# Kernel optimization log

Hardware: AMD Instinct MI355X
Metric: run time of the kernel (lower is better)

Reference implementation:

```python
import jax, jax.numpy as jnp
import numpy as np

B, QLEN, MLEN, E, H, DH = 2, 1024, 1024, 1024, 16, 64
KLEN = QLEN + MLEN
LN_EPS = 1e-3  # keras LayerNormalization default epsilon


def layer_norm(x, gamma, beta):
    mu = jnp.mean(x, axis=-1, keepdims=True)
    var = jnp.mean(jnp.square(x - mu), axis=-1, keepdims=True)
    return (x - mu) * jax.lax.rsqrt(var + LN_EPS) * gamma + beta


def rel_shift(x):
    # x: [B, H, q, k] -> standard Transformer-XL relative shift
    b, h, q, k = x.shape
    x = jnp.pad(x, ((0, 0), (0, 0), (0, 0), (1, 0)))
    x = x.reshape(b, h, k + 1, q)[:, :, 1:, :]
    return x.reshape(b, h, q, k)


def setup_inputs() -> dict:
    key = jax.random.key(0)
    ks = jax.random.split(key, 12)
    s = 0.02
    inp = {
        "w": jax.random.normal(ks[0], (B, QLEN, E), jnp.float32),
        "r": jax.random.normal(ks[1], (1, KLEN, E), jnp.float32),
        "member": jax.random.normal(ks[2], (B, MLEN, E), jnp.float32),
        # causal mask over concatenated keys: 1 = masked
        "attn_mask": (jnp.arange(KLEN)[None, :] > (jnp.arange(QLEN)[:, None] + MLEN)).astype(jnp.float32),
        "Wq": jax.random.normal(ks[3], (E, H * DH), jnp.float32) * s,
        "Wk": jax.random.normal(ks[4], (E, H * DH), jnp.float32) * s,
        "Wv": jax.random.normal(ks[5], (E, H * DH), jnp.float32) * s,
        "Wr": jax.random.normal(ks[6], (E, H * DH), jnp.float32) * s,
        "Wo": jax.random.normal(ks[7], (H * DH, E), jnp.float32) * s,
        "r_w_bias": jnp.zeros((H, DH), jnp.float32),
        "r_r_bias": jnp.zeros((H, DH), jnp.float32),
        "ln1_g": jnp.ones((E,), jnp.float32),
        "ln1_b": jnp.zeros((E,), jnp.float32),
        "W1": jax.random.normal(ks[8], (E, 4 * E), jnp.float32) * s,
        "W2": jax.random.normal(ks[9], (4 * E, E), jnp.float32) * s,
        "ln2_g": jnp.ones((E,), jnp.float32),
        "ln2_b": jnp.zeros((E,), jnp.float32),
    }
    return inp


def reference(w, r, member, attn_mask, Wq, Wk, Wv, Wr, Wo, r_w_bias, r_r_bias,
              ln1_g, ln1_b, W1, W2, ln2_g, ln2_b):
    b, qlen, e = w.shape
    h, dh = r_w_bias.shape
    cat = jnp.concatenate([member, w], axis=1)          # [B, klen, E]
    q = (cat @ Wq)[:, -qlen:]                           # [B, q, H*DH]
    k = cat @ Wk                                        # [B, klen, H*DH]
    v = cat @ Wv
    rp = (r @ Wr)[0]                                    # [klen, H*DH] (shared over batch)
    qh = q.reshape(b, qlen, h, dh)
    kh = k.reshape(b, -1, h, dh)
    vh = v.reshape(b, -1, h, dh)
    rh = rp.reshape(-1, h, dh)
    AC = jnp.einsum('bqhd,bkhd->bhqk', qh + r_w_bias, kh)
    BD = jnp.einsum('bqhd,khd->bhqk', qh + r_r_bias, rh)
    BD = rel_shift(BD)
    attn = (AC + BD) / jnp.sqrt(jnp.float32(e))         # note: scaled by sqrt(embed_size)
    m = attn_mask[None, None]                           # [1,1,q,klen]
    attn = attn * (1.0 - m) - 1e30 * m
    p = jax.nn.softmax(attn, axis=-1)
    o = jnp.einsum('bhqk,bkhd->bqhd', p, vh).reshape(b, qlen, h * dh)
    o = o @ Wo
    x = layer_norm(w + o, ln1_g, ln1_b)
    y = jax.nn.relu(x @ W1) @ W2
    return layer_norm(y + x, ln2_g, ln2_b)
```

## Files before the change

### kernel.cpp

```cpp
#include <hip/hip_runtime.h>
#include <hip/hip_bf16.h>
#include <stdint.h>

typedef __bf16 bf16x8 __attribute__((ext_vector_type(8)));
typedef float  f32x4  __attribute__((ext_vector_type(4)));

constexpr int BB   = 2;
constexpr int QL   = 1024;
constexpr int ML   = 1024;
constexpr int KL   = 2048;
constexpr int ED   = 1024;
constexpr int HH   = 16;
constexpr int FF   = 4096;
constexpr size_t MN = 2048u * 1024u;

__device__ __forceinline__ bf16x8 ld8(const __hip_bfloat16* p) {
    return *reinterpret_cast<const bf16x8*>(p);
}
__device__ __forceinline__ void st8(__hip_bfloat16* p, bf16x8 v) {
    *reinterpret_cast<bf16x8*>(p) = v;
}
__device__ __forceinline__ f32x4 mfma16(bf16x8 a, bf16x8 b, f32x4 c) {
    return __builtin_amdgcn_mfma_f32_16x16x32_bf16(a, b, c, 0, 0, 0);
}
__device__ __forceinline__ void async16(void* lds, const void* g) {
    __builtin_amdgcn_global_load_lds((__attribute__((address_space(1))) void*)g,
                                     (__attribute__((address_space(3))) void*)lds,
                                     16, 0, 0);
}

__global__ __launch_bounds__(256) void build_cat_r(const float* __restrict__ w,
                                                   const float* __restrict__ mem,
                                                   const float* __restrict__ r,
                                                   __hip_bfloat16* __restrict__ cat,
                                                   __hip_bfloat16* __restrict__ rbf) {
    const int bx = blockIdx.x;
    const float* src;
    __hip_bfloat16* dst;
    size_t g;
    if (bx < 2048) {
        size_t t = (size_t)bx * 256 + threadIdx.x;
        g = t * 8;
        int b   = (int)(g >> 21);
        int rem = (int)(g & ((1u << 21) - 1));
        int j = rem >> 10, e = rem & 1023;
        src = (j < ML) ? &mem[((size_t)b * ML + j) * ED + e]
                       : &w[((size_t)b * QL + (j - ML)) * ED + e];
        dst = &cat[g];
    } else {
        g = ((size_t)(bx - 2048) * 256 + threadIdx.x) * 8;
        src = &r[g];
        dst = &rbf[g];
    }
    float4 f0 = *(const float4*)src;
    float4 f1 = *(const float4*)(src + 4);
    union { bf16x8 v; __hip_bfloat16 h[8]; } u;
    u.h[0] = __float2bfloat16(f0.x); u.h[1] = __float2bfloat16(f0.y);
    u.h[2] = __float2bfloat16(f0.z); u.h[3] = __float2bfloat16(f0.w);
    u.h[4] = __float2bfloat16(f1.x); u.h[5] = __float2bfloat16(f1.y);
    u.h[6] = __float2bfloat16(f1.z); u.h[7] = __float2bfloat16(f1.w);
    st8(dst, u.v);
}

__global__ __launch_bounds__(256) void transpose_cast(const float* __restrict__ in,
                                                      __hip_bfloat16* __restrict__ out,
                                                      int K, int N) {
    __shared__ float tile[32][33];
    const int tx = threadIdx.x & 31, ty = threadIdx.x >> 5;
    const int n0 = blockIdx.x * 32, k0 = blockIdx.y * 32;
#pragma unroll
    for (int i = 0; i < 4; ++i)
        tile[ty + i * 8][tx] = in[(size_t)(k0 + ty + i * 8) * N + n0 + tx];
    __syncthreads();
#pragma unroll
    for (int i = 0; i < 4; ++i)
        out[(size_t)(n0 + ty + i * 8) * K + k0 + tx] = __float2bfloat16(tile[tx][ty + i * 8]);
}

__global__ __launch_bounds__(256) void tc5(const float* __restrict__ s0, const float* __restrict__ s1,
                                           const float* __restrict__ s2, const float* __restrict__ s3,
                                           const float* __restrict__ s4,
                                           __hip_bfloat16* __restrict__ wqkvT,
                                           __hip_bfloat16* __restrict__ wot) {
    __shared__ float tile[32][33];
    const int z = blockIdx.z;
    const float* in = (z == 0) ? s0 : (z == 1) ? s1 : (z == 2) ? s2 : (z == 3) ? s3 : s4;
    __hip_bfloat16* out = (z == 4) ? wot : wqkvT + (size_t)z * 1024 * 1024;
    const int tx = threadIdx.x & 31, ty = threadIdx.x >> 5;
    const int n0 = blockIdx.x * 32, k0 = blockIdx.y * 32;
#pragma unroll
    for (int i = 0; i < 4; ++i)
        tile[ty + i * 8][tx] = in[(size_t)(k0 + ty + i * 8) * 1024 + n0 + tx];
    __syncthreads();
#pragma unroll
    for (int i = 0; i < 4; ++i)
        out[(size_t)(n0 + ty + i * 8) * 1024 + k0 + tx] = __float2bfloat16(tile[tx][ty + i * 8]);
}

__global__ __launch_bounds__(256) void transpose_v(const __hip_bfloat16* __restrict__ v,
                                                   __hip_bfloat16* __restrict__ vt) {
    __shared__ __hip_bfloat16 tile[32][33];
    const int tx = threadIdx.x & 31, ty = threadIdx.x >> 5;
    const int s = blockIdx.z, b = s >> 4, h = s & 15;
    const int j0 = blockIdx.x * 32, d0 = blockIdx.y * 32;
#pragma unroll
    for (int i = 0; i < 4; ++i)
        tile[ty + i * 8][tx] =
            v[((size_t)b * KL + j0 + ty + i * 8) * 1024 + h * 64 + d0 + tx];
    __syncthreads();
#pragma unroll
    for (int i = 0; i < 4; ++i)
        vt[((size_t)s * 64 + d0 + ty + i * 8) * KL + j0 + tx] = tile[tx][ty + i * 8];
}

template <int EPI, bool SK>
__global__ __launch_bounds__(256) void gemm_bt(const __hip_bfloat16* __restrict__ A,
                                               const __hip_bfloat16* __restrict__ Bt,
                                               void* __restrict__ Cv,
                                               int N, int kLen, int lda, int ldb) {
    __shared__ __align__(16) __hip_bfloat16 sA[128 * 32];
    __shared__ __align__(16) __hip_bfloat16 sB[128 * 32];
    const int tid = threadIdx.x;
    const int lane = tid & 63;
    const int l16 = lane & 15, quad = lane >> 4;
    const int wv = tid >> 6;
    const int wm = wv >> 1, wn = wv & 1;
    const int bm = blockIdx.y * 128, bn = blockIdx.x * 128;
    const int kOff = SK ? blockIdx.z * kLen : 0;
    const int c0 = tid, c1 = 256 + tid;
    const int r0 = c0 >> 2, o0 = (c0 & 3) * 8;
    const int r1 = c1 >> 2, o1 = (c1 & 3) * 8;
    f32x4 acc[4][4] = {};
    for (int k0 = 0; k0 < kLen; k0 += 32) {
        async16(&sA[c0 * 8], A + (size_t)(bm + r0) * lda + kOff + k0 + o0);
        async16(&sA[c1 * 8], A + (size_t)(bm + r1) * lda + kOff + k0 + o1);
        async16(&sB[c0 * 8], Bt + (size_t)(bn + r0) * ldb + kOff + k0 + o0);
        async16(&sB[c1 * 8], Bt + (size_t)(bn + r1) * ldb + kOff + k0 + o1);
        __syncthreads();
        bf16x8 af[4], bfr[4];
#pragma unroll
        for (int i = 0; i < 4; ++i)
            af[i] = ld8(&sA[(wm * 64 + i * 16 + l16) * 32 + quad * 8]);
#pragma unroll
        for (int j = 0; j < 4; ++j)
            bfr[j] = ld8(&sB[(wn * 64 + j * 16 + l16) * 32 + quad * 8]);
#pragma unroll
        for (int i = 0; i < 4; ++i)
#pragma unroll
            for (int j = 0; j < 4; ++j)
                acc[i][j] = mfma16(af[i], bfr[j], acc[i][j]);
        __syncthreads();
    }
#pragma unroll
    for (int i = 0; i < 4; ++i)
#pragma unroll
        for (int j = 0; j < 4; ++j)
#pragma unroll
            for (int rg = 0; rg < 4; ++rg) {
                size_t row = bm + wm * 64 + i * 16 + quad * 4 + rg;
                size_t col = bn + wn * 64 + j * 16 + l16;
                float v = acc[i][j][rg];
                if (EPI == 0) {
                    float* C = (float*)Cv + (SK ? (size_t)blockIdx.z * MN : 0);
                    C[row * N + col] = v;
                } else {
                    __hip_bfloat16* C = (__hip_bfloat16*)Cv;
                    C[row * N + col] = __float2bfloat16(fmaxf(v, 0.f));
                }
            }
}

__global__ __launch_bounds__(256) void gemm_qkvr(const __hip_bfloat16* __restrict__ cat,
                                                 const __hip_bfloat16* __restrict__ rbf,
                                                 const __hip_bfloat16* __restrict__ Bt,
                                                 __hip_bfloat16* __restrict__ qwb,
                                                 __hip_bfloat16* __restrict__ qrb,
                                                 __hip_bfloat16* __restrict__ kbuf,
                                                 __hip_bfloat16* __restrict__ vbuf,
                                                 __hip_bfloat16* __restrict__ rpb,
                                                 const float* __restrict__ rwb,
                                                 const float* __restrict__ rrb) {
    const int id = blockIdx.x;
    int region, bm, bn;
    if (id < 128) {
        region = 0;
        int i = id, bmI = i >> 3;
        bm = (bmI >> 3) * 2048 + 1024 + (bmI & 7) * 128;
        bn = (i & 7) * 128;
    } else if (id < 384) {
        region = 1;
        int i = id - 128;
        bm = (i >> 3) * 128;
        bn = (8 + (i & 7)) * 128;
    } else if (id < 640) {
        region = 2;
        int i = id - 384;
        bm = (i >> 3) * 128;
        bn = (16 + (i & 7)) * 128;
    } else {
        region = 3;
        int i = id - 640;
        bm = (i >> 3) * 128;
        bn = (24 + (i & 7)) * 128;
    }
    const __hip_bfloat16* A = (region == 3) ? rbf : cat;
    __shared__ __align__(16) __hip_bfloat16 sA[128 * 32];
    __shared__ __align__(16) __hip_bfloat16 sB[128 * 32];
    const int tid = threadIdx.x;
    const int lane = tid & 63;
    const int l16 = lane & 15, quad = lane >> 4;
    const int wv = tid >> 6;
    const int wm = wv >> 1, wn = wv & 1;
    const int c0 = tid, c1 = 256 + tid;
    const int r0 = c0 >> 2, o0 = (c0 & 3) * 8;
    const int r1 = c1 >> 2, o1 = (c1 & 3) * 8;
    f32x4 acc[4][4] = {};
    for (int k0 = 0; k0 < 1024; k0 += 32) {
        async16(&sA[c0 * 8], A + (size_t)(bm + r0) * 1024 + k0 + o0);
        async16(&sA[c1 * 8], A + (size_t)(bm + r1) * 1024 + k0 + o1);
        async16(&sB[c0 * 8], Bt + (size_t)(bn + r0) * 1024 + k0 + o0);
        async16(&sB[c1 * 8], Bt + (size_t)(bn + r1) * 1024 + k0 + o1);
        __syncthreads();
        bf16x8 af[4], bfr[4];
#pragma unroll
        for (int i = 0; i < 4; ++i)
            af[i] = ld8(&sA[(wm * 64 + i * 16 + l16) * 32 + quad * 8]);
#pragma unroll
        for (int j = 0; j < 4; ++j)
            bfr[j] = ld8(&sB[(wn * 64 + j * 16 + l16) * 32 + quad * 8]);
#pragma unroll
        for (int i = 0; i < 4; ++i)
#pragma unroll
            for (int j = 0; j < 4; ++j)
                acc[i][j] = mfma16(af[i], bfr[j], acc[i][j]);
        __syncthreads();
    }
#pragma unroll
    for (int j = 0; j < 4; ++j) {
        const int col = bn + wn * 64 + j * 16 + l16;
        float bw = 0.f, br = 0.f;
        if (region == 0) { bw = rwb[col]; br = rrb[col]; }
#pragma unroll
        for (int i = 0; i < 4; ++i)
#pragma unroll
            for (int rg = 0; rg < 4; ++rg) {
                const int row = bm + wm * 64 + i * 16 + quad * 4 + rg;
                const int bb = row >> 11, jr = row & 2047;
                float v = acc[i][j][rg];
                if (region == 0) {
                    size_t o = ((size_t)(bb * 1024 + (jr - 1024))) * 1024 + col;
                    qwb[o] = __float2bfloat16(v + bw);
                    qrb[o] = __float2bfloat16(v + br);
                } else if (region == 1) {
                    kbuf[((size_t)(bb * 2048 + jr)) * 1024 + (col - 1024)] = __float2bfloat16(v);
                } else if (region == 2) {
                    vbuf[((size_t)(bb * 2048 + jr)) * 1024 + (col - 2048)] = __float2bfloat16(v);
                } else {
                    rpb[(size_t)row * 1024 + (col - 3072)] = __float2bfloat16(v);
                }
            }
    }
}

__global__ __launch_bounds__(128, 2) void flash_attn7(
        const __hip_bfloat16* __restrict__ qw, const __hip_bfloat16* __restrict__ qr,
        const __hip_bfloat16* __restrict__ kbuf, const __hip_bfloat16* __restrict__ vtb,
        const __hip_bfloat16* __restrict__ rpb,
        float* __restrict__ Opart, float* __restrict__ lpart) {
    __shared__ __align__(16) __hip_bfloat16 sk[64][72];
    __shared__ __align__(16) __hip_bfloat16 spb[2][32][72];
    const int tid = threadIdx.x, wv = tid >> 6, lane = tid & 63;
    const int l16 = lane & 15, quad = lane >> 4;
    const int qb = blockIdx.x >> 1, chunk = blockIdx.x & 1;
    const int h = blockIdx.y, b = blockIdx.z;
    const int i0b = qb * 64, i0w = i0b + wv * 32;

    bf16x8 qaw[2][2], qar[2][2];
#pragma unroll
    for (int g = 0; g < 2; ++g)
#pragma unroll
        for (int kf = 0; kf < 2; ++kf) {
            size_t qi = ((size_t)(b * QL + i0w + g * 16 + l16)) * 1024 + h * 64 + kf * 32 + quad * 8;
            qaw[g][kf] = ld8(&qw[qi]);
            qar[g][kf] = ld8(&qr[qi]);
        }
    f32x4 oacc[2][4] = {};
    f32x4 lacc[2] = {};
    union { bf16x8 v; __hip_bfloat16 h8[8]; } ou;
#pragma unroll
    for (int j = 0; j < 8; ++j) ou.h8[j] = __float2bfloat16(l16 == 0 ? 1.f : 0.f);
    const bf16x8 onesf = ou.v;

    int srcIdx[4], selr[4];
#pragma unroll
    for (int r = 0; r < 4; ++r) {
        int s = l16 + 15 - (quad * 4 + r);
        selr[r] = s >> 4;
        srcIdx[r] = (lane & 48) | (s & 15);
    }
    const int T = qb + 17, Ta = T >> 1;
    const int t0 = chunk ? Ta : 0, t1 = chunk ? T : Ta;
    const __hip_bfloat16* rB = rpb + h * 64;

    for (int jt = t0; jt < t1; ++jt) {
        const int j0 = jt * 64;
#pragma unroll
        for (int pp = 0; pp < 4; ++pp) {
            int cc = pp * 128 + tid, row = cc >> 3, off = (cc & 7) * 8;
            st8(&sk[row][off], ld8(&kbuf[((size_t)(b * KL + j0 + row)) * 1024 + h * 64 + off]));
        }
        bf16x8 vvf[4][2];
#pragma unroll
        for (int dt = 0; dt < 4; ++dt) {
            size_t vr = ((size_t)((b * HH + h) * 64 + dt * 16 + l16)) * 2048 + j0 + quad * 8;
            vvf[dt][0] = ld8(&vtb[vr]);
            vvf[dt][1] = ld8(&vtb[vr + 32]);
        }
        bf16x8 bF0[6], bF1[6];
        const int ubase = j0 - i0w + 992;
#pragma unroll
        for (int t = 0; t < 6; ++t) {
            int u = ubase + t * 16 + l16;
            if (u > 2047) u = 2047;
            const __hip_bfloat16* rr = rB + (size_t)u * 1024 + quad * 8;
            bF0[t] = ld8(rr);
            bF1[t] = ld8(rr + 32);
        }
        __syncthreads();
        f32x4 sfr[2][4];
#pragma unroll
        for (int nt = 0; nt < 4; ++nt) {
            bf16x8 b0 = ld8(&sk[nt * 16 + l16][quad * 8]);
            bf16x8 b1 = ld8(&sk[nt * 16 + l16][32 + quad * 8]);
#pragma unroll
            for (int g = 0; g < 2; ++g) {
                f32x4 z = {};
                z = mfma16(qaw[g][0], b0, z);
                z = mfma16(qaw[g][1], b1, z);
                sfr[g][nt] = z;
            }
        }
#pragma unroll
        for (int g = 0; g < 2; ++g) {
            f32x4 bd[5];
#pragma unroll
            for (int t = 0; t < 5; ++t) {
                int ts = t + 1 - g;
                f32x4 z = {};
                z = mfma16(qar[g][0], bF0[ts], z);
                z = mfma16(qar[g][1], bF1[ts], z);
                bd[t] = z;
            }
            float pre[5][4];
#pragma unroll
            for (int t = 0; t < 5; ++t)
#pragma unroll
                for (int r = 0; r < 4; ++r)
                    pre[t][r] = __shfl(bd[t][r], srcIdx[r], 64);
#pragma unroll
            for (int nt = 0; nt < 4; ++nt)
#pragma unroll
                for (int r = 0; r < 4; ++r) {
                    float bdv = selr[r] ? pre[nt + 1][r] : pre[nt][r];
                    float sv = (sfr[g][nt][r] + bdv) * 0.03125f;
                    int ii = i0w + g * 16 + quad * 4 + r;
                    int jj = j0 + nt * 16 + l16;
                    float p_ = (jj <= ii + ML) ? __expf(sv) : 0.f;
                    spb[wv][g * 16 + quad * 4 + r][nt * 16 + l16] = __float2bfloat16(p_);
                }
        }
#pragma unroll
        for (int g = 0; g < 2; ++g) {
            bf16x8 pa0 = ld8(&spb[wv][g * 16 + l16][quad * 8]);
            bf16x8 pa1 = ld8(&spb[wv][g * 16 + l16][32 + quad * 8]);
            lacc[g] = mfma16(pa0, onesf, lacc[g]);
            lacc[g] = mfma16(pa1, onesf, lacc[g]);
#pragma unroll
            for (int dt = 0; dt < 4; ++dt) {
                oacc[g][dt] = mfma16(pa0, vvf[dt][0], oacc[g][dt]);
                oacc[g][dt] = mfma16(pa1, vvf[dt][1], oacc[g][dt]);
            }
        }
        __syncthreads();
    }
    const size_t obase = ((size_t)((chunk * 2 + b) * HH + h)) * (1024 * 64);
#pragma unroll
    for (int g = 0; g < 2; ++g)
#pragma unroll
        for (int dt = 0; dt < 4; ++dt)
#pragma unroll
            for (int r = 0; r < 4; ++r) {
                int q = i0w + g * 16 + quad * 4 + r;
                Opart[obase + (size_t)q * 64 + dt * 16 + l16] = oacc[g][dt][r];
            }
    if (l16 == 0) {
        const size_t lbase = ((size_t)((chunk * 2 + b) * HH + h)) * 1024;
#pragma unroll
        for (int g = 0; g < 2; ++g)
#pragma unroll
            for (int r = 0; r < 4; ++r) {
                int q = i0w + g * 16 + quad * 4 + r;
                lpart[lbase + q] = lacc[g][r];
            }
    }
}

__global__ __launch_bounds__(256) void combine_attn(const float* __restrict__ Opart,
                                                    const float* __restrict__ lpart,
                                                    __hip_bfloat16* __restrict__ og) {
    size_t t = (size_t)blockIdx.x * 256 + threadIdx.x;
    size_t e4 = t * 4;
    int d  = (int)(e4 & 63);
    int q  = (int)((e4 >> 6) & 1023);
    int hh = (int)((e4 >> 16) & 15);
    int bb = (int)(e4 >> 20);
    float ox = 0.f, oy = 0.f, oz = 0.f, ow = 0.f, l = 0.f;
#pragma unroll
    for (int c = 0; c < 2; ++c) {
        size_t gsel = (size_t)((c * 2 + bb) * HH + hh);
        float4 o = *(const float4*)&Opart[gsel * (1024 * 64) + (size_t)q * 64 + d];
        ox += o.x; oy += o.y; oz += o.z; ow += o.w;
        l += lpart[gsel * 1024 + q];
    }
    float inv = 1.f / l;
    union { __hip_bfloat16 h[4]; uint2 u; } o;
    o.h[0] = __float2bfloat16(ox * inv);
    o.h[1] = __float2bfloat16(oy * inv);
    o.h[2] = __float2bfloat16(oz * inv);
    o.h[3] = __float2bfloat16(ow * inv);
    *(uint2*)&og[((size_t)bb * 1024 + q) * 1024 + hh * 64 + d] = o.u;
}

template <int NP, bool WB>
__global__ __launch_bounds__(256) void add_ln_k(const float* __restrict__ res,
                                                const float* __restrict__ parts,
                                                const float* __restrict__ gam,
                                                const float* __restrict__ bet,
                                                float* __restrict__ of,
                                                __hip_bfloat16* __restrict__ ob) {
    const int tid = threadIdx.x;
    const size_t base = (size_t)blockIdx.x * ED;
    const int col = tid * 4;
    float4 va = *(const float4*)&res[base + col];
    float x0 = va.x, x1 = va.y, x2 = va.z, x3 = va.w;
#pragma unroll
    for (int z = 0; z < NP; ++z) {
        float4 p = *(const float4*)&parts[(size_t)z * MN + base + col];
        x0 += p.x; x1 += p.y; x2 += p.z; x3 += p.w;
    }
    float s1 = x0 + x1 + x2 + x3;
    float s2 = x0 * x0 + x1 * x1 + x2 * x2 + x3 * x3;
    for (int o = 32; o > 0; o >>= 1) {
        s1 += __shfl_down(s1, o, 64);
        s2 += __shfl_down(s2, o, 64);
    }
    __shared__ float p1[4], p2[4];
    if ((tid & 63) == 0) { p1[tid >> 6] = s1; p2[tid >> 6] = s2; }
    __syncthreads();
    float S1 = p1[0] + p1[1] + p1[2] + p1[3];
    float S2 = p2[0] + p2[1] + p2[2] + p2[3];
    float mu = S1 * (1.0f / ED);
    float var = S2 * (1.0f / ED) - mu * mu;
    float rs = rsqrtf(var + 1e-3f);
    float4 g4 = *(const float4*)&gam[col];
    float4 b4 = *(const float4*)&bet[col];
    float y0 = (x0 - mu) * rs * g4.x + b4.x;
    float y1 = (x1 - mu) * rs * g4.y + b4.y;
    float y2 = (x2 - mu) * rs * g4.z + b4.z;
    float y3 = (x3 - mu) * rs * g4.w + b4.w;
    *(float4*)&of[base + col] = make_float4(y0, y1, y2, y3);
    if (WB) {
        ob[base + col + 0] = __float2bfloat16(y0);
        ob[base + col + 1] = __float2bfloat16(y1);
        ob[base + col + 2] = __float2bfloat16(y2);
        ob[base + col + 3] = __float2bfloat16(y3);
    }
}

extern "C" void kernel_launch(void* const* d_in, const int* in_sizes, int n_in,
                              void* d_out, int out_size, void* d_ws, size_t ws_size,
                              hipStream_t stream) {
    const float* w   = (const float*)d_in[0];
    const float* r   = (const float*)d_in[1];
    const float* mem = (const float*)d_in[2];
    const float* Wq  = (const float*)d_in[4];
    const float* Wk  = (const float*)d_in[5];
    const float* Wv  = (const float*)d_in[6];
    const float* Wr  = (const float*)d_in[7];
    const float* Wo  = (const float*)d_in[8];
    const float* rwb = (const float*)d_in[9];
    const float* rrb = (const float*)d_in[10];
    const float* g1  = (const float*)d_in[11];
    const float* b1  = (const float*)d_in[12];
    const float* W1  = (const float*)d_in[13];
    const float* W2  = (const float*)d_in[14];
    const float* g2  = (const float*)d_in[15];
    const float* b2  = (const float*)d_in[16];

    char* ws = (char*)d_ws;
    size_t off = 0;
    auto alloc = [&](size_t bytes) -> void* {
        void* p = ws + off;
        off += (bytes + 255) & ~(size_t)255;
        return p;
    };
    __hip_bfloat16* wqkvT = (__hip_bfloat16*)alloc((size_t)4096 * 1024 * 2);
    __hip_bfloat16* wot   = (__hip_bfloat16*)alloc((size_t)ED * ED * 2);
    __hip_bfloat16* w1t   = (__hip_bfloat16*)alloc((size_t)FF * ED * 2);
    __hip_bfloat16* w2t   = (__hip_bfloat16*)alloc((size_t)ED * FF * 2);
    __hip_bfloat16* qwb   = (__hip_bfloat16*)alloc((size_t)BB * QL * ED * 2);
    __hip_bfloat16* qrb   = (__hip_bfloat16*)alloc((size_t)BB * QL * ED * 2);
    __hip_bfloat16* vtb   = (__hip_bfloat16*)alloc((size_t)BB * KL * ED * 2);
    __hip_bfloat16* rpb   = (__hip_bfloat16*)alloc((size_t)KL * ED * 2);
    __hip_bfloat16* og    = (__hip_bfloat16*)alloc((size_t)BB * QL * ED * 2);
    char* regA = (char*)alloc((size_t)BB * KL * ED * 2);
    __hip_bfloat16* cat = (__hip_bfloat16*)regA;
    float*          xf  = (float*)regA;
    char* regB = (char*)alloc((size_t)KL * ED * 2);
    __hip_bfloat16* rbf = (__hip_bfloat16*)regB;
    __hip_bfloat16* xb  = (__hip_bfloat16*)regB;
    char* regC = (char*)alloc((size_t)BB * QL * FF * 2);
    __hip_bfloat16* kbuf = (__hip_bfloat16*)regC;
    __hip_bfloat16* vbuf = (__hip_bfloat16*)(regC + (size_t)BB * KL * ED * 2);
    __hip_bfloat16* y1   = (__hip_bfloat16*)regC;
    const size_t opartBytes = (size_t)4 * HH * QL * 64 * 4;
    const size_t lpartBytes = (size_t)4 * HH * QL * 4;
    size_t regEsz = opartBytes + lpartBytes;
    if (regEsz < (size_t)4 * MN * 4) regEsz = (size_t)4 * MN * 4;
    char* regE = (char*)alloc(regEsz);
    float* Opart  = (float*)regE;
    float* lpart  = (float*)(regE + opartBytes);
    float* o_part = (float*)regE;
    float* f_part = (float*)regE;
    if (off > ws_size) return;

    build_cat_r<<<3072, 256, 0, stream>>>(w, mem, r, cat, rbf);
    tc5<<<dim3(32, 32, 5), 256, 0, stream>>>(Wq, Wk, Wv, Wr, Wo, wqkvT, wot);
    transpose_cast<<<dim3(128, 32), 256, 0, stream>>>(W1, w1t, 1024, 4096);
    transpose_cast<<<dim3(32, 128), 256, 0, stream>>>(W2, w2t, 4096, 1024);

    gemm_qkvr<<<dim3(768), 256, 0, stream>>>(cat, rbf, wqkvT, qwb, qrb, kbuf, vbuf, rpb,
                                             rwb, rrb);
    transpose_v<<<dim3(64, 2, 32), 256, 0, stream>>>(vbuf, vtb);

    flash_attn7<<<dim3(32, 16, 2), 128, 0, stream>>>(qwb, qrb, kbuf, vtb, rpb, Opart, lpart);
    combine_attn<<<2048, 256, 0, stream>>>(Opart, lpart, og);

    gemm_bt<0, true><<<dim3(8, 16, 4), 256, 0, stream>>>(og, wot, o_part, 1024, 256, 1024, 1024);
    add_ln_k<4, true><<<2048, 256, 0, stream>>>(w, o_part, g1, b1, xf, xb);

    gemm_bt<2, false><<<dim3(32, 16, 1), 256, 0, stream>>>(xb, w1t, y1, 4096, 1024, 1024, 1024);
    gemm_bt<0, true><<<dim3(8, 16, 4), 256, 0, stream>>>(y1, w2t, f_part, 1024, 1024, 4096, 4096);
    add_ln_k<4, false><<<2048, 256, 0, stream>>>(xf, f_part, g2, b2, (float*)d_out, nullptr);
}
```

Before: 394.0 us.

## Merge weight transposes, write V transposed in QKV GEMM, split attention four ways

Three separate weight transpose-cast launches become one kernel that dispatches on block index. The V projection epilogue now writes V directly in the per-head transposed layout, which removes the transpose_v kernel and its extra read and write. Flash attention splits each query block's key range into four chunks instead of two, doubling the grid for better CU occupancy. The cost is a larger partial buffer and more work in the combine step, plus scattered, uncoalesced stores in the V epilogue.

```diff
diff --git a/kernel.cpp b/kernel.cpp
--- a/kernel.cpp
+++ b/kernel.cpp
@@ -62,12 +62,35 @@
     st8(dst, u.v);
 }
 
-__global__ __launch_bounds__(256) void transpose_cast(const float* __restrict__ in,
-                                                      __hip_bfloat16* __restrict__ out,
-                                                      int K, int N) {
+__global__ __launch_bounds__(256) void tc7(const float* __restrict__ Wq, const float* __restrict__ Wk,
+                                           const float* __restrict__ Wv, const float* __restrict__ Wr,
+                                           const float* __restrict__ Wo, const float* __restrict__ W1,
+                                           const float* __restrict__ W2,
+                                           __hip_bfloat16* __restrict__ wqkvT,
+                                           __hip_bfloat16* __restrict__ wot,
+                                           __hip_bfloat16* __restrict__ w1t,
+                                           __hip_bfloat16* __restrict__ w2t) {
     __shared__ float tile[32][33];
+    const int id = blockIdx.x;
+    const float* in;
+    __hip_bfloat16* out;
+    int K, N, k0, n0;
+    if (id < 5120) {
+        int z = id >> 10, rem = id & 1023;
+        in  = (z == 0) ? Wq : (z == 1) ? Wk : (z == 2) ? Wv : (z == 3) ? Wr : Wo;
+        out = (z == 4) ? wot : wqkvT + (size_t)z * 1024 * 1024;
+        K = 1024; N = 1024;
+        n0 = (rem & 31) * 32; k0 = (rem >> 5) * 32;
+    } else if (id < 9216) {
+        int local = id - 5120;
+        in = W1; out = w1t; K = 1024; N = 4096;
+        n0 = (local & 127) * 32; k0 = (local >> 7) * 32;
+    } else {
+        int local = id - 9216;
+        in = W2; out = w2t; K = 4096; N = 1024;
+        n0 = (local & 31) * 32; k0 = (local >> 5) * 32;
+    }
     const int tx = threadIdx.x & 31, ty = threadIdx.x >> 5;
-    const int n0 = blockIdx.x * 32, k0 = blockIdx.y * 32;
 #pragma unroll
     for (int i = 0; i < 4; ++i)
         tile[ty + i * 8][tx] = in[(size_t)(k0 + ty + i * 8) * N + n0 + tx];
@@ -75,42 +98,6 @@
 #pragma unroll
     for (int i = 0; i < 4; ++i)
         out[(size_t)(n0 + ty + i * 8) * K + k0 + tx] = __float2bfloat16(tile[tx][ty + i * 8]);
-}
-
-__global__ __launch_bounds__(256) void tc5(const float* __restrict__ s0, const float* __restrict__ s1,
-                                           const float* __restrict__ s2, const float* __restrict__ s3,
-                                           const float* __restrict__ s4,
-                                           __hip_bfloat16* __restrict__ wqkvT,
-                                           __hip_bfloat16* __restrict__ wot) {
-    __shared__ float tile[32][33];
-    const int z = blockIdx.z;
-    const float* in = (z == 0) ? s0 : (z == 1) ? s1 : (z == 2) ? s2 : (z == 3) ? s3 : s4;
-    __hip_bfloat16* out = (z == 4) ? wot : wqkvT + (size_t)z * 1024 * 1024;
-    const int tx = threadIdx.x & 31, ty = threadIdx.x >> 5;
-    const int n0 = blockIdx.x * 32, k0 = blockIdx.y * 32;
-#pragma unroll
-    for (int i = 0; i < 4; ++i)
-        tile[ty + i * 8][tx] = in[(size_t)(k0 + ty + i * 8) * 1024 + n0 + tx];
-    __syncthreads();
-#pragma unroll
-    for (int i = 0; i < 4; ++i)
-        out[(size_t)(n0 + ty + i * 8) * 1024 + k0 + tx] = __float2bfloat16(tile[tx][ty + i * 8]);
-}
-
-__global__ __launch_bounds__(256) void transpose_v(const __hip_bfloat16* __restrict__ v,
-                                                   __hip_bfloat16* __restrict__ vt) {
-    __shared__ __hip_bfloat16 tile[32][33];
-    const int tx = threadIdx.x & 31, ty = threadIdx.x >> 5;
-    const int s = blockIdx.z, b = s >> 4, h = s & 15;
-    const int j0 = blockIdx.x * 32, d0 = blockIdx.y * 32;
-#pragma unroll
-    for (int i = 0; i < 4; ++i)
-        tile[ty + i * 8][tx] =
-            v[((size_t)b * KL + j0 + ty + i * 8) * 1024 + h * 64 + d0 + tx];
-    __syncthreads();
-#pragma unroll
-    for (int i = 0; i < 4; ++i)
-        vt[((size_t)s * 64 + d0 + ty + i * 8) * KL + j0 + tx] = tile[tx][ty + i * 8];
 }
 
 template <int EPI, bool SK>
@@ -176,7 +163,7 @@
                                                  __hip_bfloat16* __restrict__ qwb,
                                                  __hip_bfloat16* __restrict__ qrb,
                                                  __hip_bfloat16* __restrict__ kbuf,
-                                                 __hip_bfloat16* __restrict__ vbuf,
+                                                 __hip_bfloat16* __restrict__ vtb,
                                                  __hip_bfloat16* __restrict__ rpb,
                                                  const float* __restrict__ rwb,
                                                  const float* __restrict__ rrb) {
@@ -254,7 +241,8 @@
                 } else if (region == 1) {
                     kbuf[((size_t)(bb * 2048 + jr)) * 1024 + (col - 1024)] = __float2bfloat16(v);
                 } else if (region == 2) {
-                    vbuf[((size_t)(bb * 2048 + jr)) * 1024 + (col - 2048)] = __float2bfloat16(v);
+                    const int cc = col - 2048, hh = cc >> 6, dd = cc & 63;
+                    vtb[(((size_t)(bb * HH + hh)) * 64 + dd) * 2048 + jr] = __float2bfloat16(v);
                 } else {
                     rpb[(size_t)row * 1024 + (col - 3072)] = __float2bfloat16(v);
                 }
@@ -262,7 +250,7 @@
     }
 }
 
-__global__ __launch_bounds__(128, 2) void flash_attn7(
+__global__ __launch_bounds__(128, 2) void flash_attn8(
         const __hip_bfloat16* __restrict__ qw, const __hip_bfloat16* __restrict__ qr,
         const __hip_bfloat16* __restrict__ kbuf, const __hip_bfloat16* __restrict__ vtb,
         const __hip_bfloat16* __restrict__ rpb,
@@ -271,7 +259,7 @@
     __shared__ __align__(16) __hip_bfloat16 spb[2][32][72];
     const int tid = threadIdx.x, wv = tid >> 6, lane = tid & 63;
     const int l16 = lane & 15, quad = lane >> 4;
-    const int qb = blockIdx.x >> 1, chunk = blockIdx.x & 1;
+    const int qb = blockIdx.x >> 2, chunk = blockIdx.x & 3;
     const int h = blockIdx.y, b = blockIdx.z;
     const int i0b = qb * 64, i0w = i0b + wv * 32;
 
@@ -298,8 +286,8 @@
         selr[r] = s >> 4;
         srcIdx[r] = (lane & 48) | (s & 15);
     }
-    const int T = qb + 17, Ta = T >> 1;
-    const int t0 = chunk ? Ta : 0, t1 = chunk ? T : Ta;
+    const int T = qb + 17;
+    const int t0 = (chunk * T) >> 2, t1 = ((chunk + 1) * T) >> 2;
     const __hip_bfloat16* rB = rpb + h * 64;
 
     for (int jt = t0; jt < t1; ++jt) {
@@ -416,7 +404,7 @@
     int bb = (int)(e4 >> 20);
     float ox = 0.f, oy = 0.f, oz = 0.f, ow = 0.f, l = 0.f;
 #pragma unroll
-    for (int c = 0; c < 2; ++c) {
+    for (int c = 0; c < 4; ++c) {
         size_t gsel = (size_t)((c * 2 + bb) * HH + hh);
         float4 o = *(const float4*)&Opart[gsel * (1024 * 64) + (size_t)q * 64 + d];
         ox += o.x; oy += o.y; oz += o.z; ow += o.w;
@@ -521,10 +509,9 @@
     __hip_bfloat16* xb  = (__hip_bfloat16*)regB;
     char* regC = (char*)alloc((size_t)BB * QL * FF * 2);
     __hip_bfloat16* kbuf = (__hip_bfloat16*)regC;
-    __hip_bfloat16* vbuf = (__hip_bfloat16*)(regC + (size_t)BB * KL * ED * 2);
     __hip_bfloat16* y1   = (__hip_bfloat16*)regC;
-    const size_t opartBytes = (size_t)4 * HH * QL * 64 * 4;
-    const size_t lpartBytes = (size_t)4 * HH * QL * 4;
+    const size_t opartBytes = (size_t)8 * HH * QL * 64 * 4;
+    const size_t lpartBytes = (size_t)8 * HH * QL * 4;
     size_t regEsz = opartBytes + lpartBytes;
     if (regEsz < (size_t)4 * MN * 4) regEsz = (size_t)4 * MN * 4;
     char* regE = (char*)alloc(regEsz);
@@ -535,15 +522,12 @@
     if (off > ws_size) return;
 
     build_cat_r<<<3072, 256, 0, stream>>>(w, mem, r, cat, rbf);
-    tc5<<<dim3(32, 32, 5), 256, 0, stream>>>(Wq, Wk, Wv, Wr, Wo, wqkvT, wot);
-    transpose_cast<<<dim3(128, 32), 256, 0, stream>>>(W1, w1t, 1024, 4096);
-    transpose_cast<<<dim3(32, 128), 256, 0, stream>>>(W2, w2t, 4096, 1024);
-
-    gemm_qkvr<<<dim3(768), 256, 0, stream>>>(cat, rbf, wqkvT, qwb, qrb, kbuf, vbuf, rpb,
+    tc7<<<13312, 256, 0, stream>>>(Wq, Wk, Wv, Wr, Wo, W1, W2, wqkvT, wot, w1t, w2t);
+
+    gemm_qkvr<<<dim3(768), 256, 0, stream>>>(cat, rbf, wqkvT, qwb, qrb, kbuf, vtb, rpb,
                                              rwb, rrb);
-    transpose_v<<<dim3(64, 2, 32), 256, 0, stream>>>(vbuf, vtb);
-
-    flash_attn7<<<dim3(32, 16, 2), 128, 0, stream>>>(qwb, qrb, kbuf, vtb, rpb, Opart, lpart);
+
+    flash_attn8<<<dim3(64, 16, 2), 128, 0, stream>>>(qwb, qrb, kbuf, vtb, rpb, Opart, lpart);
     combine_attn<<<2048, 256, 0, stream>>>(Opart, lpart, og);
 
     gemm_bt<0, true><<<dim3(8, 16, 4), 256, 0, stream>>>(og, wot, o_part, 1024, 256, 1024, 1024);
```

Result: no change. 390.8 us (-0.8%).
